# Kernel optimization log

Measured on AMD Instinct MI355X. Metric: run time of the kernel, lower is better.

Reference implementation:

```python
import jax, jax.numpy as jnp
import numpy as np

N = 1_000_000        # points
V = 200_000          # occupied voxels
B = 4                # scans per batch
NUM_CLASSES = 20
DIM_POINT = 4
EPS = 1e-5


def bn(x, g, b):
    # eval-mode BatchNorm1d with running_mean=0, running_var=1
    return x * (g / jnp.sqrt(1.0 + EPS)) + b


def _lin(key, fi, fo):
    # kaiming-normal init, bias-free Linear stored as [in, out]
    return jax.random.normal(key, (fi, fo), jnp.float32) * np.sqrt(2.0 / fi)


def setup_inputs() -> dict:
    key = jax.random.key(0)
    ks = jax.random.split(key, 20)
    batch_ids = (jnp.arange(N) * B // N).astype(jnp.float32)[:, None]
    coords = jax.random.normal(ks[0], (N, DIM_POINT), jnp.float32)
    points = jnp.concatenate([batch_ids, coords], axis=1)           # [N, 1+dim_point]
    pv_ids = jax.random.randint(ks[1], (N,), 0, V, jnp.int64)       # point -> voxel
    ones, zeros = jnp.ones, jnp.zeros
    return {
        'points': points, 'point_voxel_ids': pv_ids,
        # point encoder: 4->32->64->32, each Linear(no bias)+BN+ReLU
        'pe_w1': _lin(ks[2], DIM_POINT, 32), 'pe_g1': ones(32), 'pe_b1': zeros(32),
        'pe_w2': _lin(ks[3], 32, 64),        'pe_g2': ones(64), 'pe_b2': zeros(64),
        'pe_w3': _lin(ks[4], 64, 32),        'pe_g3': ones(32), 'pe_b3': zeros(32),
        # voxel encoder (SparseUnet simplified to per-voxel 32->32->32)
        've_w1': _lin(ks[5], 32, 32), 've_g1': ones(32), 've_b1': zeros(32),
        've_w2': _lin(ks[6], 32, 32), 've_g2': ones(32), 've_b2': zeros(32),
        # fusion encoder: 64->64
        'fu_w': _lin(ks[7], 64, 64), 'fu_g': ones(64), 'fu_b': zeros(64),
        # FlattenSELayer: 64 -> 64//16 -> 64 with biases
        'se_w1': _lin(ks[8], 64, 4),  'se_b1': zeros(4),
        'se_w2': _lin(ks[9], 4, 64),  'se_b2': zeros(64),
        # main classifier 64->32->num_classes
        'cls_w1': _lin(ks[10], 64, 32), 'cls_g1': ones(32), 'cls_b1': zeros(32),
        'cls_w2': _lin(ks[11], 32, NUM_CLASSES),
        # aux classifier 32->32->num_classes
        'aux_w1': _lin(ks[12], 32, 32), 'aux_g1': ones(32), 'aux_b1': zeros(32),
        'aux_w2': _lin(ks[13], 32, NUM_CLASSES),
    }


def reference(points, point_voxel_ids,
              pe_w1, pe_g1, pe_b1, pe_w2, pe_g2, pe_b2, pe_w3, pe_g3, pe_b3,
              ve_w1, ve_g1, ve_b1, ve_w2, ve_g2, ve_b2,
              fu_w, fu_g, fu_b, se_w1, se_b1, se_w2, se_b2,
              cls_w1, cls_g1, cls_b1, cls_w2,
              aux_w1, aux_g1, aux_b1, aux_w2):
    batch_ids = points[:, 0].astype(jnp.int32)
    pv = point_voxel_ids.astype(jnp.int32)
    x = points[:, 1:]
    # point encoder
    pf = jax.nn.relu(bn(x @ pe_w1, pe_g1, pe_b1))
    pf = jax.nn.relu(bn(pf @ pe_w2, pe_g2, pe_b2))
    pf = jax.nn.relu(bn(pf @ pe_w3, pe_g3, pe_b3))               # [N,32]
    # voxel_max_pooling: point -> voxel scatter-max (empty voxels -> 0)
    vox = jax.ops.segment_max(pf, pv, num_segments=V)
    vox = jnp.where(jnp.isfinite(vox), vox, 0.0)                 # [V,32]
    # voxel encoder (SparseUnet stand-in); v1 is the aux feature tap
    v1 = jax.nn.relu(bn(vox @ ve_w1, ve_g1, ve_b1))              # [V,32]
    vf = jax.nn.relu(bn(v1 @ ve_w2, ve_g2, ve_b2))               # [V,32]
    # voxel_to_point gather + fusion
    pvf = vf[pv]                                                  # [N,32]
    fused = jnp.concatenate([pvf, pf], axis=1)                   # [N,64]
    fused = jax.nn.relu(bn(fused @ fu_w, fu_g, fu_b))
    # FlattenSELayer: per-scan mean -> gate -> residual scale
    sums = jax.ops.segment_sum(fused, batch_ids, num_segments=B)
    cnts = jax.ops.segment_sum(jnp.ones((fused.shape[0], 1), fused.dtype), batch_ids, num_segments=B)
    mean = sums / jnp.maximum(cnts, 1.0)                         # [B,64]
    gate = jax.nn.sigmoid(jax.nn.relu(mean @ se_w1 + se_b1) @ se_w2 + se_b2)
    fused = fused + fused * gate[batch_ids]
    # heads (dropout is identity at inference)
    out = jax.nn.relu(bn(fused @ cls_w1, cls_g1, cls_b1)) @ cls_w2      # [N,C]
    aux_out = jax.nn.relu(bn(v1 @ aux_w1, aux_g1, aux_b1)) @ aux_w2     # [V,C]
    return out, aux_out
```

## Files before the change

### kernel.cpp

```cpp
#include <hip/hip_runtime.h>
#include <hip/hip_bf16.h>

#define NPTS 1000000
#define NVOX 200000
#define NCLS 20

typedef __hip_bfloat16 bf16;
typedef __attribute__((ext_vector_type(8))) short bf16x8_t;
typedef __attribute__((ext_vector_type(4))) float f32x4_t;
#define MFMA16(a, b, c) __builtin_amdgcn_mfma_f32_16x16x32_bf16(a, b, c, 0, 0, 0)

constexpr size_t L_PTSC = 0;
constexpr size_t L_PV   = L_PTSC + (size_t)NPTS * 4;
constexpr size_t L_BID  = L_PV + NPTS;
constexpr size_t L_CNT  = L_BID + NPTS;
constexpr size_t L_BSUM = L_CNT + NVOX;
constexpr size_t L_BCNT = L_BSUM + 2048;
constexpr size_t L_GATE = L_BCNT + 4;
constexpr size_t L_FLAG = L_GATE + 256;
constexpr size_t L_OFFS = L_FLAG + 4;
constexpr size_t L_OFFW = L_OFFS + NVOX;
constexpr size_t L_BS1  = L_OFFW + NVOX;
constexpr size_t L_BB   = L_BS1 + 256;
constexpr size_t L_IDX  = L_BB + 256;
constexpr size_t L_W    = L_IDX + NPTS;
constexpr int O_PE1W = 0;      constexpr int O_PE1B = 128;
constexpr int O_PE2W = 160;    constexpr int O_PE2B = 2208;
constexpr int O_PE3W = 2272;   constexpr int O_PE3B = 4320;
constexpr int O_VE1W = 4352;   constexpr int O_VE1B = 5376;
constexpr int O_VE2W = 5408;   constexpr int O_VE2B = 6432;
constexpr int O_FUW  = 6464;   constexpr int O_FUB  = 10560;
constexpr int O_SE1W = 10624;  constexpr int O_SE1B = 10880;
constexpr int O_SE2W = 10884;  constexpr int O_SE2B = 11140;
constexpr int O_CLS1W = 11204; constexpr int O_CLS1B = 13252;
constexpr int O_CLS2W = 13284;
constexpr int O_AUX1W = 13924; constexpr int O_AUX1B = 14948;
constexpr int O_AUX2W = 14980;
constexpr int W_TOTAL = 15620;
constexpr size_t L_WT  = L_W + W_TOTAL;
static_assert((L_WT * 4) % 16 == 0, "WT alignment");
constexpr int WT_FU = 0;
constexpr int WT_C1 = 4096;
constexpr int WT_C2 = 6144;
constexpr int WT_2H = 7168;
constexpr int WT_2L = 9216;
constexpr int WT_3H = 11264;
constexpr int WT_3L = 13312;
constexpr int WT_C1B = 15360;
constexpr int WT_U16 = 15360 + 8192;
constexpr size_t L_VFU = L_WT + WT_U16 / 2;
constexpr size_t L_PFQ = L_VFU + (size_t)NVOX * 16;
constexpr size_t L_PFS = L_PFQ + (size_t)NPTS * 16;
static_assert((L_VFU * 4) % 16 == 0, "vf alignment");
static_assert((L_PFQ * 4) % 16 == 0, "pf alignment");
static_assert((L_PFS * 4) % 16 == 0, "pfs alignment");

static __device__ __forceinline__ float b2f(bf16 v) { return __bfloat162float(v); }
static __device__ __forceinline__ float us2f(unsigned short u) { return __uint_as_float((unsigned)u << 16); }
static __device__ __forceinline__ unsigned short f2us(float f) {
    unsigned u = __float_as_uint(f);
    u += 0x7fffu + ((u >> 16) & 1u);
    return (unsigned short)(u >> 16);
}
static __device__ __forceinline__ unsigned pack2(float a, float b) {
    return (unsigned)f2us(a) | ((unsigned)f2us(b) << 16);
}
static __device__ __forceinline__ void unpack2(unsigned u, float& a, float& b) {
    a = __uint_as_float(u << 16);
    b = __uint_as_float(u & 0xffff0000u);
}
static __device__ __forceinline__ float rdf(const void* p, size_t idx, int fp32) {
    return fp32 ? ((const float*)p)[idx] : b2f(((const bf16*)p)[idx]);
}
static __device__ __forceinline__ int detect_fp32(const void* pts_raw) {
    const unsigned short* ptsu = (const unsigned short*)pts_raw;
    return (ptsu[1] == 0 && ptsu[11] == 0) ? 1 : 0;
}
static __device__ __forceinline__ int detect_i64(const void* pv_raw) {
    const unsigned* pvu = (const unsigned*)pv_raw;
    return (pvu[1] == 0 && pvu[3] == 0 && pvu[5] == 0 && pvu[7] == 0) ? 1 : 0;
}

template <int K, int M, bool RELU, bool BIAS>
static __device__ __forceinline__ void dense(const float* __restrict__ x, float* __restrict__ y,
                                             const float* __restrict__ w, const float* __restrict__ b) {
#pragma unroll
    for (int j = 0; j < M; ++j) {
        float a = BIAS ? b[j] : 0.f;
#pragma unroll
        for (int k = 0; k < K; ++k) a = fmaf(x[k], w[k * M + j], a);
        y[j] = RELU ? fmaxf(a, 0.f) : a;
    }
}

static __device__ __forceinline__ int block_excl_scan(int v, int t) {
    __shared__ int sh[2][256];
    int cur = 0;
    sh[0][t] = v; __syncthreads();
#pragma unroll
    for (int off = 1; off < 256; off <<= 1) {
        int val = sh[cur][t];
        if (t >= off) val += sh[cur][t - off];
        sh[cur ^ 1][t] = val; __syncthreads();
        cur ^= 1;
    }
    return sh[cur][t] - v;
}

struct WPtrs {
    const void *pe_w1, *pe_g1, *pe_b1, *pe_w2, *pe_g2, *pe_b2, *pe_w3, *pe_g3, *pe_b3;
    const void *ve_w1, *ve_g1, *ve_b1, *ve_w2, *ve_g2, *ve_b2;
    const void *fu_w, *fu_g, *fu_b;
    const void *se_w1, *se_b1, *se_w2, *se_b2;
    const void *cls_w1, *cls_g1, *cls_b1, *cls_w2;
    const void *aux_w1, *aux_g1, *aux_b1, *aux_w2;
};

static __device__ void foldw(float* d, const void* w, const void* g, int K, int M, int fp32) {
    const float INV = 0.9999950000374997f;
    for (int idx = threadIdx.x; idx < K * M; idx += 256)
        d[idx] = rdf(w, idx, fp32) * (rdf(g, idx % M, fp32) * INV);
}
static __device__ void cpv(float* d, const void* s, int n, int fp32) {
    for (int idx = threadIdx.x; idx < n; idx += 256) d[idx] = rdf(s, idx, fp32);
}

__global__ void k0_prep(WPtrs p, const void* __restrict__ pts_raw, float* __restrict__ W,
                        unsigned short* __restrict__ WT) {
    int f = detect_fp32(pts_raw);
    foldw(W + O_PE1W, p.pe_w1, p.pe_g1, 4, 32, f);   cpv(W + O_PE1B, p.pe_b1, 32, f);
    foldw(W + O_PE2W, p.pe_w2, p.pe_g2, 32, 64, f);  cpv(W + O_PE2B, p.pe_b2, 64, f);
    foldw(W + O_PE3W, p.pe_w3, p.pe_g3, 64, 32, f);  cpv(W + O_PE3B, p.pe_b3, 32, f);
    foldw(W + O_VE1W, p.ve_w1, p.ve_g1, 32, 32, f);  cpv(W + O_VE1B, p.ve_b1, 32, f);
    foldw(W + O_VE2W, p.ve_w2, p.ve_g2, 32, 32, f);  cpv(W + O_VE2B, p.ve_b2, 32, f);
    foldw(W + O_FUW,  p.fu_w,  p.fu_g,  64, 64, f);  cpv(W + O_FUB,  p.fu_b, 64, f);
    cpv(W + O_SE1W, p.se_w1, 256, f);  cpv(W + O_SE1B, p.se_b1, 4, f);
    cpv(W + O_SE2W, p.se_w2, 256, f);  cpv(W + O_SE2B, p.se_b2, 64, f);
    foldw(W + O_CLS1W, p.cls_w1, p.cls_g1, 64, 32, f); cpv(W + O_CLS1B, p.cls_b1, 32, f);
    cpv(W + O_CLS2W, p.cls_w2, 640, f);
    foldw(W + O_AUX1W, p.aux_w1, p.aux_g1, 32, 32, f); cpv(W + O_AUX1B, p.aux_b1, 32, f);
    cpv(W + O_AUX2W, p.aux_w2, 640, f);
    __syncthreads();
    unsigned short* wtfu = WT + WT_FU;
    unsigned short* wtc1 = WT + WT_C1;
    unsigned short* wtc2 = WT + WT_C2;
    unsigned short* wt2h = WT + WT_2H;
    unsigned short* wt2l = WT + WT_2L;
    unsigned short* wt3h = WT + WT_3H;
    unsigned short* wt3l = WT + WT_3L;
    for (int idx = threadIdx.x; idx < 4096; idx += 256) {
        int n = idx >> 6, k = idx & 63;
        wtfu[idx] = f2us(W[O_FUW + k * 64 + n]);
    }
    for (int idx = threadIdx.x; idx < 2048; idx += 256) {
        int n = idx >> 6, k = idx & 63;
        wtc1[idx] = f2us(W[O_CLS1W + k * 32 + n]);
    }
    for (int idx = threadIdx.x; idx < 1024; idx += 256) {
        int n = idx >> 5, k = idx & 31;
        wtc2[idx] = (n < NCLS) ? f2us(W[O_CLS2W + k * NCLS + n]) : (unsigned short)0;
    }
    for (int idx = threadIdx.x; idx < 2048; idx += 256) {
        int n = idx >> 5, k = idx & 31;
        float v = W[O_PE2W + k * 64 + n];
        unsigned short hi = f2us(v);
        wt2h[idx] = hi;
        wt2l[idx] = f2us(v - us2f(hi));
    }
    for (int idx = threadIdx.x; idx < 2048; idx += 256) {
        int n = idx >> 6, k = idx & 63;
        float v = W[O_PE3W + k * 32 + n];
        unsigned short hi = f2us(v);
        wt3h[idx] = hi;
        wt3l[idx] = f2us(v - us2f(hi));
    }
}

__global__ __launch_bounds__(256) void k_scan1(const int* __restrict__ cnt, int* __restrict__ bs) {
    int t = threadIdx.x;
    int base = blockIdx.x * 1024 + t * 4;
    int s = 0;
#pragma unroll
    for (int k = 0; k < 4; ++k) { int idx = base + k; if (idx < NVOX) s += cnt[idx]; }
    __shared__ int red[256];
    red[t] = s; __syncthreads();
    for (int off = 128; off > 0; off >>= 1) { if (t < off) red[t] += red[t + off]; __syncthreads(); }
    if (t == 0) bs[blockIdx.x] = red[0];
}

__global__ __launch_bounds__(256) void k_scan2(const int* __restrict__ bs, int* __restrict__ bb, int nb) {
    int t = threadIdx.x;
    int v = (t < nb) ? bs[t] : 0;
    int e = block_excl_scan(v, t);
    bb[t] = e;
}

__global__ __launch_bounds__(256) void k_scan3(const int* __restrict__ cnt, const int* __restrict__ bb,
                                               int* __restrict__ offs) {
    int t = threadIdx.x;
    int base = blockIdx.x * 1024 + t * 4;
    int c[4]; int s = 0;
#pragma unroll
    for (int k = 0; k < 4; ++k) { int idx = base + k; c[k] = (idx < NVOX) ? cnt[idx] : 0; s += c[k]; }
    int run = bb[blockIdx.x] + block_excl_scan(s, t);
#pragma unroll
    for (int k = 0; k < 4; ++k) {
        int idx = base + k;
        if (idx < NVOX) { offs[idx] = run; run += c[k]; }
    }
}

__global__ __launch_bounds__(256) void k1_fused(const void* __restrict__ pts_raw,
                                                const void* __restrict__ pv_raw,
                                                const float* __restrict__ W,
                                                const unsigned short* __restrict__ WT2H,
                                                const unsigned short* __restrict__ WT2L,
                                                const unsigned short* __restrict__ WT3H,
                                                const unsigned short* __restrict__ WT3L,
                                                int* __restrict__ pvN,
                                                int* __restrict__ bidN,
                                                int* __restrict__ cnt,
                                                float* __restrict__ bcnt,
                                                int* __restrict__ rank,
                                                uint4* __restrict__ pf_q) {
    __shared__ __align__(16) unsigned short hth[4][16][72];
    __shared__ __align__(16) unsigned short htl[4][16][72];
    __shared__ __align__(16) unsigned short pt[4][16][40];
    int t = threadIdx.x;
    int lane = t & 63, w = t >> 6;
    int m = lane & 15, quad = lane >> 4;
    int i0 = blockIdx.x * 256;
    int fp32 = detect_fp32(pts_raw), i64 = detect_i64(pv_raw);

    float w1[32], b1[8];
#pragma unroll
    for (int k = 0; k < 4; ++k)
#pragma unroll
        for (int j = 0; j < 8; ++j) w1[k * 8 + j] = W[O_PE1W + k * 32 + quad * 8 + j];
#pragma unroll
    for (int j = 0; j < 8; ++j) b1[j] = W[O_PE1B + quad * 8 + j];
    bf16x8_t b2h[4], b2l[4], b3h[2][2], b3l[2][2];
    float bias2[4], bias3[2];
#pragma unroll
    for (int tn = 0; tn < 4; ++tn) {
        b2h[tn] = *(const bf16x8_t*)(WT2H + (tn * 16 + m) * 32 + quad * 8);
        b2l[tn] = *(const bf16x8_t*)(WT2L + (tn * 16 + m) * 32 + quad * 8);
        bias2[tn] = W[O_PE2B + tn * 16 + m];
    }
#pragma unroll
    for (int tn = 0; tn < 2; ++tn) {
#pragma unroll
        for (int kh = 0; kh < 2; ++kh) {
            b3h[tn][kh] = *(const bf16x8_t*)(WT3H + (tn * 16 + m) * 64 + kh * 32 + quad * 8);
            b3l[tn][kh] = *(const bf16x8_t*)(WT3L + (tn * 16 + m) * 64 + kh * 32 + quad * 8);
        }
        bias3[tn] = W[O_PE3B + tn * 16 + m];
    }
    int nval = NPTS - i0; if (nval > 256) nval = 256;
    int ntiles = (nval - w * 64 >= 64) ? 4 : 0;

#pragma unroll 1
    for (int tt = 0; tt < ntiles; ++tt) {
        int rbase = i0 + w * 64 + tt * 16;
        int arow = rbase + m;
        float4 c;
        c.x = rdf(pts_raw, (size_t)arow * 5 + 1, fp32);
        c.y = rdf(pts_raw, (size_t)arow * 5 + 2, fp32);
        c.z = rdf(pts_raw, (size_t)arow * 5 + 3, fp32);
        c.w = rdf(pts_raw, (size_t)arow * 5 + 4, fp32);
        union { unsigned u[4]; bf16x8_t v; } ah, al;
#pragma unroll
        for (int pp = 0; pp < 4; ++pp) {
            unsigned hu = 0, lu = 0;
#pragma unroll
            for (int s = 0; s < 2; ++s) {
                int j = 2 * pp + s;
                float h = b1[j];
                h = fmaf(c.x, w1[0 * 8 + j], h);
                h = fmaf(c.y, w1[1 * 8 + j], h);
                h = fmaf(c.z, w1[2 * 8 + j], h);
                h = fmaf(c.w, w1[3 * 8 + j], h);
                h = fmaxf(h, 0.f);
                unsigned short hi = f2us(h);
                unsigned short lo = f2us(h - us2f(hi));
                hu |= (unsigned)hi << (16 * s);
                lu |= (unsigned)lo << (16 * s);
            }
            ah.u[pp] = hu; al.u[pp] = lu;
        }
#pragma unroll
        for (int tn = 0; tn < 4; ++tn) {
            f32x4_t acc = {0.f, 0.f, 0.f, 0.f};
            acc = MFMA16(ah.v, b2h[tn], acc);
            acc = MFMA16(ah.v, b2l[tn], acc);
            acc = MFMA16(al.v, b2h[tn], acc);
#pragma unroll
            for (int e = 0; e < 4; ++e) {
                float v = fmaxf(acc[e] + bias2[tn], 0.f);
                unsigned short hi = f2us(v);
                hth[w][quad * 4 + e][tn * 16 + m] = hi;
                htl[w][quad * 4 + e][tn * 16 + m] = f2us(v - us2f(hi));
            }
        }
        bf16x8_t x0h = *(const bf16x8_t*)&hth[w][m][quad * 8];
        bf16x8_t x1h = *(const bf16x8_t*)&hth[w][m][32 + quad * 8];
        bf16x8_t x0l = *(const bf16x8_t*)&htl[w][m][quad * 8];
        bf16x8_t x1l = *(const bf16x8_t*)&htl[w][m][32 + quad * 8];
#pragma unroll
        for (int tn = 0; tn < 2; ++tn) {
            f32x4_t acc = {0.f, 0.f, 0.f, 0.f};
            acc = MFMA16(x0h, b3h[tn][0], acc);
            acc = MFMA16(x1h, b3h[tn][1], acc);
            acc = MFMA16(x0h, b3l[tn][0], acc);
            acc = MFMA16(x1h, b3l[tn][1], acc);
            acc = MFMA16(x0l, b3h[tn][0], acc);
            acc = MFMA16(x1l, b3h[tn][1], acc);
#pragma unroll
            for (int e = 0; e < 4; ++e)
                pt[w][quad * 4 + e][tn * 16 + m] = f2us(fmaxf(acc[e] + bias3[tn], 0.f));
        }
        uint4 q = *(const uint4*)&pt[w][m][quad * 8];
        pf_q[(size_t)arow * 4 + quad] = q;
    }

    int i = i0 + t;
    bool valid = t < nval;
    int b = 0, rk = 0;
    if (valid) {
        b = (int)rdf(pts_raw, (size_t)i * 5, fp32);
        bidN[i] = b;
        int v = i64 ? (int)((const long long*)pv_raw)[i] : ((const int*)pv_raw)[i];
        pvN[i] = v;
        rk = atomicAdd(&cnt[v], 1);
    }
    __shared__ int sb0, sflag;
    if (t == 0) { sb0 = b; sflag = 1; }
    __syncthreads();
    if (valid && b != sb0) sflag = 0;
    __syncthreads();
    if (sflag) {
        if (t == 0) atomicAdd(&bcnt[sb0], (float)nval);
    } else if (valid) {
        atomicAdd(&bcnt[b], 1.f);
    }
    if (valid) rank[i] = rk;
}

__global__ __launch_bounds__(256) void k_scat(const int* __restrict__ pv,
                                              const int* __restrict__ rank,
                                              const int* __restrict__ offs,
                                              const uint4* __restrict__ pf_q,
                                              uint4* __restrict__ pf_s) {
    int tid = blockIdx.x * 256 + threadIdx.x;
    int i = tid >> 2, quad = tid & 3;
    if (i >= NPTS) return;
    int sp = offs[pv[i]] + rank[i];
    pf_s[(size_t)sp * 4 + quad] = pf_q[(size_t)i * 4 + quad];
}

__global__ __launch_bounds__(256) void k_voxmlp(const int* __restrict__ offs, const int* __restrict__ cnt,
                                                const uint4* __restrict__ pf_s,
                                                const float* __restrict__ W,
                                                const void* __restrict__ pts_raw,
                                                unsigned* __restrict__ vf_u,
                                                void* __restrict__ outbase) {
    int v = blockIdx.x * 256 + threadIdx.x;
    if (v >= NVOX) return;
    int of32 = detect_fp32(pts_raw);
    float mx[32];
#pragma unroll
    for (int c = 0; c < 32; ++c) mx[c] = 0.f;
    int s = offs[v], n = cnt[v];
    for (int p = 0; p < n; ++p) {
        size_t base = (size_t)(s + p) * 4;
#pragma unroll
        for (int t = 0; t < 4; ++t) {
            uint4 q = pf_s[base + t];
            float a, b;
            unpack2(q.x, a, b); mx[8*t+0] = fmaxf(mx[8*t+0], a); mx[8*t+1] = fmaxf(mx[8*t+1], b);
            unpack2(q.y, a, b); mx[8*t+2] = fmaxf(mx[8*t+2], a); mx[8*t+3] = fmaxf(mx[8*t+3], b);
            unpack2(q.z, a, b); mx[8*t+4] = fmaxf(mx[8*t+4], a); mx[8*t+5] = fmaxf(mx[8*t+5], b);
            unpack2(q.w, a, b); mx[8*t+6] = fmaxf(mx[8*t+6], a); mx[8*t+7] = fmaxf(mx[8*t+7], b);
        }
    }
    float v1[32], vf[32], a1[32], o[20];
    dense<32, 32, true, true>(mx, v1, W + O_VE1W, W + O_VE1B);
    dense<32, 32, true, true>(v1, vf, W + O_VE2W, W + O_VE2B);
#pragma unroll
    for (int c = 0; c < 16; ++c) vf_u[(size_t)v * 16 + c] = pack2(vf[2*c], vf[2*c+1]);
    dense<32, 32, true, true>(v1, a1, W + O_AUX1W, W + O_AUX1B);
    dense<32, 20, false, false>(a1, o, W + O_AUX2W, nullptr);
    if (of32) {
        float* auxf = (float*)outbase + (size_t)NPTS * NCLS + (size_t)v * NCLS;
#pragma unroll
        for (int t = 0; t < NCLS; ++t) __builtin_nontemporal_store(o[t], auxf + t);
    } else {
        unsigned* auxu = (unsigned*)((bf16*)outbase + (size_t)NPTS * NCLS);
#pragma unroll
        for (int t = 0; t < 10; ++t) __builtin_nontemporal_store(pack2(o[2*t], o[2*t+1]), auxu + (size_t)v * 10 + t);
    }
}

__global__ __launch_bounds__(256) void k3_mfma(const int* __restrict__ bid, const int* __restrict__ pv,
                                               const uint4* __restrict__ pf_q,
                                               const uint4* __restrict__ vf_q,
                                               const float* __restrict__ W,
                                               const unsigned short* __restrict__ WTfu,
                                               float* __restrict__ bsum8) {
    __shared__ int sbid[256];
    __shared__ float red[4][64];
    __shared__ int sflag;
    int t = threadIdx.x;
    int i0 = blockIdx.x * 256;
    int nval = NPTS - i0; if (nval > 256) nval = 256;
    if (t < nval) sbid[t] = bid[i0 + t];
    if (t == 0) sflag = (bid[i0] == bid[i0 + nval - 1]) ? 1 : 0;

    int lane = t & 63, w = t >> 6;
    int m = lane & 15, quad = lane >> 4;
    bf16x8_t bw0[4], bw1[4];
    float bias[4];
#pragma unroll
    for (int tn = 0; tn < 4; ++tn) {
        bw0[tn] = *(const bf16x8_t*)(WTfu + (tn * 16 + m) * 64 + quad * 8);
        bw1[tn] = *(const bf16x8_t*)(WTfu + (tn * 16 + m) * 64 + 32 + quad * 8);
        bias[tn] = W[O_FUB + tn * 16 + m];
    }
    __syncthreads();
    int uni = sflag;
    int b0 = sbid[0];
    int rep = (blockIdx.x & 7) * 256;
    int ntiles = (nval - w * 64 >= 64) ? 4 : 0;

    float csum[4] = {0.f, 0.f, 0.f, 0.f};
#pragma unroll
    for (int tt = 0; tt < 4; ++tt) {
        if (tt >= ntiles) break;
        int rbase = i0 + w * 64 + tt * 16;
        int arow = rbase + m;
        int pvr = pv[arow];
        uint4 va = vf_q[(size_t)pvr * 4 + quad];
        uint4 vb = pf_q[(size_t)arow * 4 + quad];
        bf16x8_t a0 = *(bf16x8_t*)&va;
        bf16x8_t a1 = *(bf16x8_t*)&vb;
        float f[4][4];
#pragma unroll
        for (int tn = 0; tn < 4; ++tn) {
            f32x4_t acc = {0.f, 0.f, 0.f, 0.f};
            acc = MFMA16(a0, bw0[tn], acc);
            acc = MFMA16(a1, bw1[tn], acc);
#pragma unroll
            for (int e = 0; e < 4; ++e) f[tn][e] = fmaxf(acc[e] + bias[tn], 0.f);
        }
        if (uni) {
#pragma unroll
            for (int tn = 0; tn < 4; ++tn) {
                float s = f[tn][0] + f[tn][1] + f[tn][2] + f[tn][3];
                s += __shfl_xor(s, 16);
                s += __shfl_xor(s, 32);
                csum[tn] += s;
            }
        } else {
#pragma unroll
            for (int tn = 0; tn < 4; ++tn)
#pragma unroll
                for (int e = 0; e < 4; ++e)
                    atomicAdd(&bsum8[rep + sbid[rbase - i0 + quad * 4 + e] * 64 + tn * 16 + m], f[tn][e]);
        }
    }
    if (uni) {
        float mine = quad == 0 ? csum[0] : quad == 1 ? csum[1] : quad == 2 ? csum[2] : csum[3];
        red[w][quad * 16 + m] = mine;
        __syncthreads();
        if (t < 64) {
            float s = red[0][t] + red[1][t] + red[2][t] + red[3][t];
            atomicAdd(&bsum8[rep + b0 * 64 + t], s);
        }
    }
}

__global__ void k4_gate(const float* __restrict__ bsum8, const float* __restrict__ bcnt,
                        const float* __restrict__ W, const unsigned short* __restrict__ WTc1,
                        float* __restrict__ gate, unsigned short* __restrict__ WTc1B) {
    __shared__ float m[4][64];
    __shared__ float hid[4][4];
    __shared__ float gl[256];
    int tid = threadIdx.x, b = tid >> 6, c = tid & 63;
    float s = 0.f;
#pragma unroll
    for (int r = 0; r < 8; ++r) s += bsum8[r * 256 + tid];
    m[b][c] = s / fmaxf(bcnt[b], 1.f);
    __syncthreads();
    if (c < 4) {
        const float* w = W + O_SE1W;
        float a = (W + O_SE1B)[c];
        for (int k = 0; k < 64; ++k) a = fmaf(m[b][k], w[k * 4 + c], a);
        hid[b][c] = fmaxf(a, 0.f);
    }
    __syncthreads();
    const float* w2 = W + O_SE2W;
    float g = (W + O_SE2B)[c];
#pragma unroll
    for (int h = 0; h < 4; ++h) g = fmaf(hid[b][h], w2[h * 64 + c], g);
    g = 1.f + 1.f / (1.f + expf(-g));
    gate[tid] = g;
    gl[tid] = g;
    __syncthreads();
    for (int idx = tid; idx < 8192; idx += 256) {
        int bb = idx >> 11, j = idx & 2047, k = j & 63;
        WTc1B[idx] = f2us(us2f(WTc1[j]) * gl[bb * 64 + k]);
    }
}

__global__ __launch_bounds__(256) void k5_mfma(const int* __restrict__ bid, const int* __restrict__ pv,
                                               const uint4* __restrict__ pf_q,
                                               const uint4* __restrict__ vf_q,
                                               const float* __restrict__ W,
                                               const unsigned short* __restrict__ WTfu,
                                               const unsigned short* __restrict__ WTc1,
                                               const unsigned short* __restrict__ WTc1B,
                                               const unsigned short* __restrict__ WTc2,
                                               const float* __restrict__ gate,
                                               const void* __restrict__ pts_raw,
                                               void* __restrict__ out) {
    __shared__ float sg[256];
    __shared__ int sbid[256];
    __shared__ int sflag;
    __shared__ __align__(16) unsigned short ft[4][16][72];
    __shared__ __align__(16) unsigned short ht[4][16][40];
    __shared__ float ot[4][16][20];
    int t = threadIdx.x;
    int i0 = blockIdx.x * 256;
    int nval = NPTS - i0; if (nval > 256) nval = 256;
    sg[t] = gate[t];
    if (t < nval) sbid[t] = bid[i0 + t];
    if (t == 0) sflag = (bid[i0] == bid[i0 + nval - 1]) ? 1 : 0;

    int lane = t & 63, w = t >> 6;
    int m = lane & 15, quad = lane >> 4;
    bf16x8_t bfu0[4], bfu1[4];
    float biasfu[4];
#pragma unroll
    for (int tn = 0; tn < 4; ++tn) {
        bfu0[tn] = *(const bf16x8_t*)(WTfu + (tn * 16 + m) * 64 + quad * 8);
        bfu1[tn] = *(const bf16x8_t*)(WTfu + (tn * 16 + m) * 64 + 32 + quad * 8);
        biasfu[tn] = W[O_FUB + tn * 16 + m];
    }
    __syncthreads();
    int uni = sflag;
    int b0 = sbid[0];
    int of32 = detect_fp32(pts_raw);
    int ntiles = (nval - w * 64 >= 64) ? 4 : 0;

    const unsigned short* c1base = uni ? (WTc1B + b0 * 2048) : WTc1;
    bf16x8_t bc10[2], bc11[2], bc2[2];
    float biasc1[2];
#pragma unroll
    for (int tn = 0; tn < 2; ++tn) {
        bc10[tn] = *(const bf16x8_t*)(c1base + (tn * 16 + m) * 64 + quad * 8);
        bc11[tn] = *(const bf16x8_t*)(c1base + (tn * 16 + m) * 64 + 32 + quad * 8);
        bc2[tn]  = *(const bf16x8_t*)(WTc2 + (tn * 16 + m) * 32 + quad * 8);
        biasc1[tn] = W[O_CLS1B + tn * 16 + m];
    }

#pragma unroll 1
    for (int tt = 0; tt < ntiles; ++tt) {
        int rbase = i0 + w * 64 + tt * 16;
        int arow = rbase + m;
        int pvr = pv[arow];
        uint4 va = vf_q[(size_t)pvr * 4 + quad];
        uint4 vb = pf_q[(size_t)arow * 4 + quad];
        bf16x8_t a0 = *(bf16x8_t*)&va;
        bf16x8_t a1 = *(bf16x8_t*)&vb;
#pragma unroll
        for (int tn = 0; tn < 4; ++tn) {
            f32x4_t acc = {0.f, 0.f, 0.f, 0.f};
            acc = MFMA16(a0, bfu0[tn], acc);
            acc = MFMA16(a1, bfu1[tn], acc);
#pragma unroll
            for (int e = 0; e < 4; ++e) {
                float fv = fmaxf(acc[e] + biasfu[tn], 0.f);
                if (!uni) fv *= sg[sbid[rbase - i0 + quad * 4 + e] * 64 + tn * 16 + m];
                ft[w][quad * 4 + e][tn * 16 + m] = f2us(fv);
            }
        }
        bf16x8_t c0 = *(const bf16x8_t*)&ft[w][m][quad * 8];
        bf16x8_t c1 = *(const bf16x8_t*)&ft[w][m][32 + quad * 8];
#pragma unroll
        for (int tn = 0; tn < 2; ++tn) {
            f32x4_t acc = {0.f, 0.f, 0.f, 0.f};
            acc = MFMA16(c0, bc10[tn], acc);
            acc = MFMA16(c1, bc11[tn], acc);
#pragma unroll
            for (int e = 0; e < 4; ++e)
                ht[w][quad * 4 + e][tn * 16 + m] = f2us(fmaxf(acc[e] + biasc1[tn], 0.f));
        }
        bf16x8_t d0 = *(const bf16x8_t*)&ht[w][m][quad * 8];
#pragma unroll
        for (int tn = 0; tn < 2; ++tn) {
            f32x4_t acc = {0.f, 0.f, 0.f, 0.f};
            acc = MFMA16(d0, bc2[tn], acc);
            int c = tn * 16 + m;
            if (c < NCLS) {
#pragma unroll
                for (int e = 0; e < 4; ++e) ot[w][quad * 4 + e][c] = acc[e];
            }
        }
        if (of32) {
            float* of = (float*)out + (size_t)rbase * NCLS;
#pragma unroll
            for (int k = 0; k < 5; ++k) {
                int idx = k * 64 + lane;
                __builtin_nontemporal_store(((const float*)ot[w])[idx], of + idx);
            }
        } else {
            unsigned* ow = (unsigned*)((unsigned short*)out + (size_t)rbase * NCLS);
#pragma unroll
            for (int k = 0; k < 3; ++k) {
                int idx = k * 64 + lane;
                if (idx < 160) {
                    int p = idx / 10, c2 = idx - p * 10;
                    __builtin_nontemporal_store(pack2(ot[w][p][2 * c2], ot[w][p][2 * c2 + 1]), ow + idx);
                }
            }
        }
    }
}

extern "C" void kernel_launch(void* const* d_in, const int* in_sizes, int n_in,
                              void* d_out, int out_size, void* d_ws, size_t ws_size,
                              hipStream_t stream) {
    WPtrs p;
    p.pe_w1 = d_in[2];  p.pe_g1 = d_in[3];  p.pe_b1 = d_in[4];
    p.pe_w2 = d_in[5];  p.pe_g2 = d_in[6];  p.pe_b2 = d_in[7];
    p.pe_w3 = d_in[8];  p.pe_g3 = d_in[9];  p.pe_b3 = d_in[10];
    p.ve_w1 = d_in[11]; p.ve_g1 = d_in[12]; p.ve_b1 = d_in[13];
    p.ve_w2 = d_in[14]; p.ve_g2 = d_in[15]; p.ve_b2 = d_in[16];
    p.fu_w  = d_in[17]; p.fu_g  = d_in[18]; p.fu_b  = d_in[19];
    p.se_w1 = d_in[20]; p.se_b1 = d_in[21];
    p.se_w2 = d_in[22]; p.se_b2 = d_in[23];
    p.cls_w1 = d_in[24]; p.cls_g1 = d_in[25]; p.cls_b1 = d_in[26];
    p.cls_w2 = d_in[27];
    p.aux_w1 = d_in[28]; p.aux_g1 = d_in[29]; p.aux_b1 = d_in[30];
    p.aux_w2 = d_in[31];

    float* base = (float*)d_ws;
    int*   pvN  = (int*)(base + L_PV);
    int*   bidN = (int*)(base + L_BID);
    int*   cnt  = (int*)(base + L_CNT);
    float* bsum8 = base + L_BSUM;
    float* bcnt = base + L_BCNT;
    float* gate = base + L_GATE;
    int*   offs = (int*)(base + L_OFFS);
    int*   bs1  = (int*)(base + L_BS1);
    int*   bb   = (int*)(base + L_BB);
    int*   rank = (int*)(base + L_IDX);
    float* W    = base + L_W;
    unsigned short* WT = (unsigned short*)(base + L_WT);
    unsigned short* wtfu = WT + WT_FU;
    unsigned short* wtc1 = WT + WT_C1;
    unsigned short* wtc2 = WT + WT_C2;
    unsigned short* wt2h = WT + WT_2H;
    unsigned short* wt2l = WT + WT_2L;
    unsigned short* wt3h = WT + WT_3H;
    unsigned short* wt3l = WT + WT_3L;
    unsigned short* wtc1b = WT + WT_C1B;
    unsigned* vf_u = (unsigned*)(base + L_VFU);
    uint4* pf_q = (uint4*)(base + L_PFQ);
    uint4* pf_s = (uint4*)(base + L_PFS);

    constexpr int NBV = (NVOX + 255) / 256;
    constexpr int NBS = (NVOX + 1023) / 1024;
    constexpr int NBM = (NPTS + 255) / 256;
    constexpr int NBSC = (NPTS * 4 + 255) / 256;

    hipMemsetAsync(cnt, 0, (NVOX + 2048 + 4) * sizeof(float), stream);
    k0_prep<<<1, 256, 0, stream>>>(p, d_in[0], W, WT);
    k1_fused<<<NBM, 256, 0, stream>>>(d_in[0], d_in[1], W, wt2h, wt2l, wt3h, wt3l,
                                      pvN, bidN, cnt, bcnt, rank, pf_q);
    k_scan1<<<NBS, 256, 0, stream>>>(cnt, bs1);
    k_scan2<<<1, 256, 0, stream>>>(bs1, bb, NBS);
    k_scan3<<<NBS, 256, 0, stream>>>(cnt, bb, offs);
    k_scat<<<NBSC, 256, 0, stream>>>(pvN, rank, offs, pf_q, pf_s);
    k_voxmlp<<<NBV, 256, 0, stream>>>(offs, cnt, pf_s, W, d_in[0], vf_u, d_out);
    k3_mfma<<<NBM, 256, 0, stream>>>(bidN, pvN, pf_q, (const uint4*)vf_u, W, wtfu, bsum8);
    k4_gate<<<1, 256, 0, stream>>>(bsum8, bcnt, W, wtc1, gate, wtc1b);
    k5_mfma<<<NBM, 256, 0, stream>>>(bidN, pvN, pf_q, (const uint4*)vf_u, W,
                                     wtfu, wtc1, wtc1b, wtc2, gate, d_in[0], d_out);
}
```

Measured before the change: 553.9 us.

## Scatter voxel features to per-point buffer to remove gathers in fusion kernels

```diff
diff --git a/kernel.cpp b/kernel.cpp
--- a/kernel.cpp
+++ b/kernel.cpp
@@ -10,20 +10,18 @@
 typedef __attribute__((ext_vector_type(4))) float f32x4_t;
 #define MFMA16(a, b, c) __builtin_amdgcn_mfma_f32_16x16x32_bf16(a, b, c, 0, 0, 0)
 
-constexpr size_t L_PTSC = 0;
-constexpr size_t L_PV   = L_PTSC + (size_t)NPTS * 4;
+constexpr size_t L_PV   = 0;
 constexpr size_t L_BID  = L_PV + NPTS;
 constexpr size_t L_CNT  = L_BID + NPTS;
 constexpr size_t L_BSUM = L_CNT + NVOX;
 constexpr size_t L_BCNT = L_BSUM + 2048;
 constexpr size_t L_GATE = L_BCNT + 4;
-constexpr size_t L_FLAG = L_GATE + 256;
-constexpr size_t L_OFFS = L_FLAG + 4;
-constexpr size_t L_OFFW = L_OFFS + NVOX;
-constexpr size_t L_BS1  = L_OFFW + NVOX;
+constexpr size_t L_OFFS = L_GATE + 256;
+constexpr size_t L_BS1  = L_OFFS + NVOX;
 constexpr size_t L_BB   = L_BS1 + 256;
 constexpr size_t L_IDX  = L_BB + 256;
-constexpr size_t L_W    = L_IDX + NPTS;
+constexpr size_t L_IOR  = L_IDX + NPTS;
+constexpr size_t L_W    = L_IOR + NPTS;
 constexpr int O_PE1W = 0;      constexpr int O_PE1B = 128;
 constexpr int O_PE2W = 160;    constexpr int O_PE2B = 2208;
 constexpr int O_PE3W = 2272;   constexpr int O_PE3B = 4320;
@@ -38,7 +36,6 @@
 constexpr int O_AUX2W = 14980;
 constexpr int W_TOTAL = 15620;
 constexpr size_t L_WT  = L_W + W_TOTAL;
-static_assert((L_WT * 4) % 16 == 0, "WT alignment");
 constexpr int WT_FU = 0;
 constexpr int WT_C1 = 4096;
 constexpr int WT_C2 = 6144;
@@ -48,12 +45,12 @@
 constexpr int WT_3L = 13312;
 constexpr int WT_C1B = 15360;
 constexpr int WT_U16 = 15360 + 8192;
-constexpr size_t L_VFU = L_WT + WT_U16 / 2;
-constexpr size_t L_PFQ = L_VFU + (size_t)NVOX * 16;
+constexpr size_t L_PFQ = L_WT + WT_U16 / 2;
 constexpr size_t L_PFS = L_PFQ + (size_t)NPTS * 16;
-static_assert((L_VFU * 4) % 16 == 0, "vf alignment");
-static_assert((L_PFQ * 4) % 16 == 0, "pf alignment");
+constexpr size_t L_VFP = L_PFS + (size_t)NPTS * 16;
+static_assert((L_PFQ * 4) % 16 == 0, "pfq alignment");
 static_assert((L_PFS * 4) % 16 == 0, "pfs alignment");
+static_assert((L_VFP * 4) % 16 == 0, "vfp alignment");
 
 static __device__ __forceinline__ float b2f(bf16 v) { return __bfloat162float(v); }
 static __device__ __forceinline__ float us2f(unsigned short u) { return __uint_as_float((unsigned)u << 16); }
@@ -350,19 +347,22 @@
                                               const int* __restrict__ rank,
                                               const int* __restrict__ offs,
                                               const uint4* __restrict__ pf_q,
-                                              uint4* __restrict__ pf_s) {
+                                              uint4* __restrict__ pf_s,
+                                              int* __restrict__ iorig) {
     int tid = blockIdx.x * 256 + threadIdx.x;
     int i = tid >> 2, quad = tid & 3;
     if (i >= NPTS) return;
     int sp = offs[pv[i]] + rank[i];
     pf_s[(size_t)sp * 4 + quad] = pf_q[(size_t)i * 4 + quad];
+    if (quad == 0) iorig[sp] = i;
 }
 
 __global__ __launch_bounds__(256) void k_voxmlp(const int* __restrict__ offs, const int* __restrict__ cnt,
                                                 const uint4* __restrict__ pf_s,
+                                                const int* __restrict__ iorig,
                                                 const float* __restrict__ W,
                                                 const void* __restrict__ pts_raw,
-                                                unsigned* __restrict__ vf_u,
+                                                uint4* __restrict__ vfp,
                                                 void* __restrict__ outbase) {
     int v = blockIdx.x * 256 + threadIdx.x;
     if (v >= NVOX) return;
@@ -386,8 +386,16 @@
     float v1[32], vf[32], a1[32], o[20];
     dense<32, 32, true, true>(mx, v1, W + O_VE1W, W + O_VE1B);
     dense<32, 32, true, true>(v1, vf, W + O_VE2W, W + O_VE2B);
-#pragma unroll
-    for (int c = 0; c < 16; ++c) vf_u[(size_t)v * 16 + c] = pack2(vf[2*c], vf[2*c+1]);
+    uint4 vq[4];
+#pragma unroll
+    for (int t = 0; t < 4; ++t)
+        vq[t] = make_uint4(pack2(vf[8*t+0], vf[8*t+1]), pack2(vf[8*t+2], vf[8*t+3]),
+                           pack2(vf[8*t+4], vf[8*t+5]), pack2(vf[8*t+6], vf[8*t+7]));
+    for (int p = 0; p < n; ++p) {
+        int orig = iorig[s + p];
+        uint4* d = vfp + (size_t)orig * 4;
+        d[0] = vq[0]; d[1] = vq[1]; d[2] = vq[2]; d[3] = vq[3];
+    }
     dense<32, 32, true, true>(v1, a1, W + O_AUX1W, W + O_AUX1B);
     dense<32, 20, false, false>(a1, o, W + O_AUX2W, nullptr);
     if (of32) {
@@ -401,9 +409,9 @@
     }
 }
 
-__global__ __launch_bounds__(256) void k3_mfma(const int* __restrict__ bid, const int* __restrict__ pv,
+__global__ __launch_bounds__(256) void k3_mfma(const int* __restrict__ bid,
                                                const uint4* __restrict__ pf_q,
-                                               const uint4* __restrict__ vf_q,
+                                               const uint4* __restrict__ vfp,
                                                const float* __restrict__ W,
                                                const unsigned short* __restrict__ WTfu,
                                                float* __restrict__ bsum8) {
@@ -438,8 +446,7 @@
         if (tt >= ntiles) break;
         int rbase = i0 + w * 64 + tt * 16;
         int arow = rbase + m;
-        int pvr = pv[arow];
-        uint4 va = vf_q[(size_t)pvr * 4 + quad];
+        uint4 va = vfp[(size_t)arow * 4 + quad];
         uint4 vb = pf_q[(size_t)arow * 4 + quad];
         bf16x8_t a0 = *(bf16x8_t*)&va;
         bf16x8_t a1 = *(bf16x8_t*)&vb;
@@ -512,9 +519,9 @@
     }
 }
 
-__global__ __launch_bounds__(256) void k5_mfma(const int* __restrict__ bid, const int* __restrict__ pv,
+__global__ __launch_bounds__(256) void k5_mfma(const int* __restrict__ bid,
                                                const uint4* __restrict__ pf_q,
-                                               const uint4* __restrict__ vf_q,
+                                               const uint4* __restrict__ vfp,
                                                const float* __restrict__ W,
                                                const unsigned short* __restrict__ WTfu,
                                                const unsigned short* __restrict__ WTc1,
@@ -567,8 +574,7 @@
     for (int tt = 0; tt < ntiles; ++tt) {
         int rbase = i0 + w * 64 + tt * 16;
         int arow = rbase + m;
-        int pvr = pv[arow];
-        uint4 va = vf_q[(size_t)pvr * 4 + quad];
+        uint4 va = vfp[(size_t)arow * 4 + quad];
         uint4 vb = pf_q[(size_t)arow * 4 + quad];
         bf16x8_t a0 = *(bf16x8_t*)&va;
         bf16x8_t a1 = *(bf16x8_t*)&vb;
@@ -655,6 +661,7 @@
     int*   bs1  = (int*)(base + L_BS1);
     int*   bb   = (int*)(base + L_BB);
     int*   rank = (int*)(base + L_IDX);
+    int*   iorig = (int*)(base + L_IOR);
     float* W    = base + L_W;
     unsigned short* WT = (unsigned short*)(base + L_WT);
     unsigned short* wtfu = WT + WT_FU;
@@ -665,9 +672,9 @@
     unsigned short* wt3h = WT + WT_3H;
     unsigned short* wt3l = WT + WT_3L;
     unsigned short* wtc1b = WT + WT_C1B;
-    unsigned* vf_u = (unsigned*)(base + L_VFU);
     uint4* pf_q = (uint4*)(base + L_PFQ);
     uint4* pf_s = (uint4*)(base + L_PFS);
+    uint4* vfp  = (uint4*)(base + L_VFP);
 
     constexpr int NBV = (NVOX + 255) / 256;
     constexpr int NBS = (NVOX + 1023) / 1024;
@@ -681,10 +688,10 @@
     k_scan1<<<NBS, 256, 0, stream>>>(cnt, bs1);
     k_scan2<<<1, 256, 0, stream>>>(bs1, bb, NBS);
     k_scan3<<<NBS, 256, 0, stream>>>(cnt, bb, offs);
-    k_scat<<<NBSC, 256, 0, stream>>>(pvN, rank, offs, pf_q, pf_s);
-    k_voxmlp<<<NBV, 256, 0, stream>>>(offs, cnt, pf_s, W, d_in[0], vf_u, d_out);
-    k3_mfma<<<NBM, 256, 0, stream>>>(bidN, pvN, pf_q, (const uint4*)vf_u, W, wtfu, bsum8);
+    k_scat<<<NBSC, 256, 0, stream>>>(pvN, rank, offs, pf_q, pf_s, iorig);
+    k_voxmlp<<<NBV, 256, 0, stream>>>(offs, cnt, pf_s, iorig, W, d_in[0], vfp, d_out);
+    k3_mfma<<<NBM, 256, 0, stream>>>(bidN, pf_q, vfp, W, wtfu, bsum8);
     k4_gate<<<1, 256, 0, stream>>>(bsum8, bcnt, W, wtc1, gate, wtc1b);
-    k5_mfma<<<NBM, 256, 0, stream>>>(bidN, pvN, pf_q, (const uint4*)vf_u, W,
+    k5_mfma<<<NBM, 256, 0, stream>>>(bidN, pf_q, vfp, W,
                                      wtfu, wtc1, wtc1b, wtc2, gate, d_in[0], d_out);
 }
```

Result: slower. 582.5 us (+5.1%).
